# Kernel optimization log

Hardware: AMD Instinct MI355X
Metric: run time of the kernel (lower is better)

## Reference

```python
import jax, jax.numpy as jnp
import numpy as np

N_V, N_E, N_F = 6000, 12000, 8000
D_IN, D_OUT = 32, 32


def _glorot(key, shape):
    lim = float(np.sqrt(6.0 / (shape[0] + shape[1])))
    return jax.random.uniform(key, shape, jnp.float32, -lim, lim)


def setup_inputs() -> dict:
    key = jax.random.key(0)
    ks = jax.random.split(key, 13)
    return {
        "xv": jax.random.normal(ks[0], (N_V, D_IN), jnp.float32),
        "xe": jax.random.normal(ks[1], (N_E, D_IN), jnp.float32),
        "xf": jax.random.normal(ks[2], (N_F, D_IN), jnp.float32),
        "Gv2v": jax.random.normal(ks[3], (N_V, N_V), jnp.float32) / np.sqrt(N_V),
        "Gv2e": jax.random.normal(ks[4], (N_E, N_V), jnp.float32) / np.sqrt(N_V),
        "Ge2e": jax.random.normal(ks[5], (N_E, N_E), jnp.float32) / np.sqrt(N_E),
        "Ge2f": jax.random.normal(ks[6], (N_F, N_E), jnp.float32) / np.sqrt(N_E),
        "Gf2f": jax.random.normal(ks[7], (N_F, N_F), jnp.float32) / np.sqrt(N_F),
        "Wv2v": _glorot(ks[8], (D_IN, D_OUT)),
        "Wv2e": _glorot(ks[9], (D_IN, D_OUT)),
        "We2e": _glorot(ks[10], (D_IN, D_OUT)),
        "We2f": _glorot(ks[11], (D_IN, D_OUT)),
        "Wf2f": _glorot(ks[12], (D_IN, D_OUT)),
    }


def reference(xv, xe, xf, Gv2v, Gv2e, Ge2e, Ge2f, Gf2f,
              Wv2v, Wv2e, We2e, We2f, Wf2f):
    # Eval mode: dropout is identity. activation=None -> no nonlinearity.
    # LTN(x, G) = G @ (x @ W); MergeOper = sum of two LTNs.
    zv = Gv2v @ (xv @ Wv2v)                               # [n_v, d_out]
    ze = Gv2e @ (xv @ Wv2e) + Ge2e @ (xe @ We2e)          # [n_e, d_out]
    zf = Ge2f @ (xe @ We2f) + Gf2f @ (xf @ Wf2f)          # [n_f, d_out]
    return zv, ze, zf
```

## Files before the change

kernel.cpp:

```cpp
#include <hip/hip_runtime.h>

typedef float  f32x4 __attribute__((ext_vector_type(4)));
typedef short  s16x8 __attribute__((ext_vector_type(8)));

#define PK   256
#define PSTR 260

typedef const __attribute__((address_space(1))) float* gas1f;
typedef __attribute__((address_space(3))) float*       las3f;

__device__ __forceinline__ short f2bf(float f) {
  unsigned u = __builtin_bit_cast(unsigned, f);
  u += 0x7FFFu + ((u >> 16) & 1u);
  return (short)(u >> 16);
}

__global__ __launch_bounds__(256) void build_yt(
    const float* __restrict__ xv, const float* __restrict__ xe,
    const float* __restrict__ xf,
    const float* __restrict__ Wv2v, const float* __restrict__ Wv2e,
    const float* __restrict__ We2e, const float* __restrict__ We2f,
    const float* __restrict__ Wf2f, short* __restrict__ Yt)
{
  int bid = blockIdx.x;
  const float* x; const float* W; int K, Kpad; size_t yoff;
  if (bid < 24)       { x=xv; W=Wv2v; K=6000;  Kpad=6144;  yoff=0;       }
  else if (bid < 48)  { x=xv; W=Wv2e; K=6000;  Kpad=6144;  yoff=196608;  bid-=24; }
  else if (bid < 95)  { x=xe; W=We2e; K=12000; Kpad=12032; yoff=393216;  bid-=48; }
  else if (bid < 142) { x=xe; W=We2f; K=12000; Kpad=12032; yoff=778240;  bid-=95; }
  else                { x=xf; W=Wf2f; K=8000;  Kpad=8192;  yoff=1163264; bid-=142; }

  __shared__ float Wl[32][32];
  int tid = threadIdx.x;
  #pragma unroll
  for (int i = 0; i < 4; ++i) {
    int e = tid + i * 256;
    Wl[e >> 5][e & 31] = W[e];
  }
  __syncthreads();

  int row = bid * 256 + tid;
  if (row >= Kpad) return;

  float acc[32];
  #pragma unroll
  for (int c = 0; c < 32; ++c) acc[c] = 0.f;

  if (row < K) {
    const float* xp = x + (size_t)row * 32;
    float xr[32];
    #pragma unroll
    for (int i = 0; i < 8; ++i) {
      f32x4 v = *(const f32x4*)(xp + i * 4);
      xr[i*4+0] = v.x; xr[i*4+1] = v.y; xr[i*4+2] = v.z; xr[i*4+3] = v.w;
    }
    #pragma unroll
    for (int d = 0; d < 32; ++d) {
      float xd = xr[d];
      #pragma unroll
      for (int c = 0; c < 32; ++c) acc[c] += xd * Wl[d][c];
    }
  }
  #pragma unroll
  for (int c = 0; c < 32; ++c)
    Yt[yoff + (size_t)c * Kpad + row] = f2bf(acc[c]);
}

__device__ __forceinline__ void stage_panel(
    const float* __restrict__ G, int K, int row0, int pn, int lane, int w,
    float (*panel)[16][PSTR], int bb)
{
  if ((pn + 1) * PK <= K) {
    const float* base = G + (size_t)row0 * K + (size_t)pn * PK;
    #pragma unroll
    for (int j = 0; j < 4; ++j) {
      int rr = 4 * w + j;
      __builtin_amdgcn_global_load_lds((gas1f)(base + (size_t)rr * K + lane * 4),
                                       (las3f)&panel[bb][rr][0], 16, 0, 2 );
    }
  } else {
    #pragma unroll
    for (int j = 0; j < 4; ++j) {
      int rr = 4 * w + j;
      int k = pn * PK + lane * 4;
      f32x4 v = {0.f, 0.f, 0.f, 0.f};
      if (k < K) v = *(const f32x4*)(G + (size_t)(row0 + rr) * K + k);
      *(f32x4*)&panel[bb][rr][lane * 4] = v;
    }
  }
}

__device__ __forceinline__ void seg_run(
    const float* __restrict__ G, const short* __restrict__ Yt,
    int K, int Kpad, int row0, int lane, int w,
    float (*panel)[16][PSTR], f32x4& acc0, f32x4& acc1)
{
  int np = (K + PK - 1) / PK;
  int r = lane & 15, g = lane >> 4;

  stage_panel(G, K, row0, 0, lane, w, panel, 0);
  stage_panel(G, K, row0, 1, lane, w, panel, 1);

  for (int p = 0; p < np; ++p) {
    if (p + 1 < np && (p + 2) * PK <= K)
      asm volatile("s_waitcnt vmcnt(4)" ::: "memory");
    else
      asm volatile("s_waitcnt vmcnt(0)" ::: "memory");
    __builtin_amdgcn_s_barrier();

    int b = p & 1;
    #pragma unroll
    for (int si = 0; si < 2; ++si) {
      int s  = 2 * w + si;
      int kk = s * 32 + g * 8;
      f32x4 a0 = *(const f32x4*)&panel[b][r][kk];
      f32x4 a1 = *(const f32x4*)&panel[b][r][kk + 4];
      s16x8 a;
      a[0] = f2bf(a0.x); a[1] = f2bf(a0.y); a[2] = f2bf(a0.z); a[3] = f2bf(a0.w);
      a[4] = f2bf(a1.x); a[5] = f2bf(a1.y); a[6] = f2bf(a1.z); a[7] = f2bf(a1.w);
      int kg = p * PK + kk;
      s16x8 vb0 = *(const s16x8*)(Yt + (size_t)r * Kpad + kg);
      s16x8 vb1 = *(const s16x8*)(Yt + (size_t)(r + 16) * Kpad + kg);
      acc0 = __builtin_amdgcn_mfma_f32_16x16x32_bf16(a, vb0, acc0, 0, 0, 0);
      acc1 = __builtin_amdgcn_mfma_f32_16x16x32_bf16(a, vb1, acc1, 0, 0, 0);
    }

    asm volatile("s_waitcnt lgkmcnt(0)" ::: "memory");
    __builtin_amdgcn_sched_barrier(0);
    __builtin_amdgcn_s_barrier();
    if (p + 2 < np) stage_panel(G, K, row0, p + 2, lane, w, panel, b);
  }
  __syncthreads();
}

__global__ __launch_bounds__(256) void gemm_skinny(
    const float* __restrict__ Gv2v, const float* __restrict__ Gv2e,
    const float* __restrict__ Ge2e, const float* __restrict__ Ge2f,
    const float* __restrict__ Gf2f, const short* __restrict__ Yt,
    float* __restrict__ out)
{
  __shared__ float panel[2][16][PSTR];

  int bid  = blockIdx.x;
  int lane = threadIdx.x & 63, w = threadIdx.x >> 6;

  const float *G0, *G1; const short *Y0, *Y1;
  int K0, Kp0, K1, Kp1, tile; size_t ob;
  if (bid < 500) {
    tile = bid;
    G0 = Ge2f; Y0 = Yt + 778240;  K0 = 12000; Kp0 = 12032;
    G1 = Gf2f; Y1 = Yt + 1163264; K1 = 8000;  Kp1 = 8192;
    ob = (size_t)18000 * 32;
  } else if (bid < 1250) {
    tile = bid - 500;
    G0 = Gv2e; Y0 = Yt + 196608;  K0 = 6000;  Kp0 = 6144;
    G1 = Ge2e; Y1 = Yt + 393216;  K1 = 12000; Kp1 = 12032;
    ob = (size_t)6000 * 32;
  } else {
    tile = bid - 1250;
    G0 = Gv2v; Y0 = Yt;           K0 = 6000;  Kp0 = 6144;
    G1 = nullptr; Y1 = nullptr;   K1 = 0; Kp1 = 0;
    ob = 0;
  }
  int row0 = tile * 16;

  f32x4 acc0 = {0.f,0.f,0.f,0.f}, acc1 = {0.f,0.f,0.f,0.f};
  seg_run(G0, Y0, K0, Kp0, row0, lane, w, panel, acc0, acc1);
  if (G1) seg_run(G1, Y1, K1, Kp1, row0, lane, w, panel, acc0, acc1);

  float (*red)[512] = (float (*)[512])panel;
  int r = lane & 15, g = lane >> 4;
  #pragma unroll
  for (int q = 0; q < 4; ++q) {
    int rw = g * 4 + q;
    red[w][rw * 32 + r]      = acc0[q];
    red[w][rw * 32 + 16 + r] = acc1[q];
  }
  __syncthreads();
  #pragma unroll
  for (int i = 0; i < 2; ++i) {
    int e = (int)threadIdx.x + i * 256;
    float s = red[0][e] + red[1][e] + red[2][e] + red[3][e];
    out[ob + (size_t)row0 * 32 + e] = s;
  }
}

extern "C" void kernel_launch(void* const* d_in, const int* in_sizes, int n_in,
                              void* d_out, int out_size, void* d_ws, size_t ws_size,
                              hipStream_t stream) {
  const float* xv   = (const float*)d_in[0];
  const float* xe   = (const float*)d_in[1];
  const float* xf   = (const float*)d_in[2];
  const float* Gv2v = (const float*)d_in[3];
  const float* Gv2e = (const float*)d_in[4];
  const float* Ge2e = (const float*)d_in[5];
  const float* Ge2f = (const float*)d_in[6];
  const float* Gf2f = (const float*)d_in[7];
  const float* Wv2v = (const float*)d_in[8];
  const float* Wv2e = (const float*)d_in[9];
  const float* We2e = (const float*)d_in[10];
  const float* We2f = (const float*)d_in[11];
  const float* Wf2f = (const float*)d_in[12];
  short* Yt  = (short*)d_ws;
  float* out = (float*)d_out;

  hipLaunchKernelGGL(build_yt, dim3(174), dim3(256), 0, stream,
                     xv, xe, xf, Wv2v, Wv2e, We2e, We2f, Wf2f, Yt);
  hipLaunchKernelGGL(gemm_skinny, dim3(1625), dim3(256), 0, stream,
                     Gv2v, Gv2e, Ge2e, Ge2f, Gf2f, Yt, out);
}
```

Measured before the change: 356.3 us.

## Double row tile to 32 with 8 waves and prefetch B fragments a panel ahead

The skinny GEMM now gives each block 32 output rows and 512 threads, so each of the eight waves owns one 32-wide k-slice of the panel and reuses its B (Yt) fragments across two 16-row MFMA tiles. This halves the number of Yt reads from global/L2 per G row and halves the block count. B fragments for the next panel are loaded into registers one iteration ahead so they overlap the barrier and staging. The final Gv2v tile is clamped so it overlaps the previous one and rewrites identical rows. Larger blocks use more LDS and registers, which may lower occupancy, and the kernel stays dominated by streaming the fp32 G matrices.

```diff
diff --git a/kernel.cpp b/kernel.cpp
--- a/kernel.cpp
+++ b/kernel.cpp
@@ -5,6 +5,7 @@
 
 #define PK   256
 #define PSTR 260
+#define TM   32
 
 typedef const __attribute__((address_space(1))) float* gas1f;
 typedef __attribute__((address_space(3))) float*       las3f;
@@ -68,7 +69,7 @@
 
 __device__ __forceinline__ void stage_panel(
     const float* __restrict__ G, int K, int row0, int pn, int lane, int w,
-    float (*panel)[16][PSTR], int bb)
+    float (*panel)[TM][PSTR], int bb)
 {
   if ((pn + 1) * PK <= K) {
     const float* base = G + (size_t)row0 * K + (size_t)pn * PK;
@@ -90,16 +91,26 @@
   }
 }
 
+__device__ __forceinline__ void loadB(const short* __restrict__ Y, int Kp,
+                                      int r, int g, int w, int p, s16x8 B[2])
+{
+  int kg = p * PK + w * 32 + g * 8;
+  B[0] = *(const s16x8*)(Y + (size_t)r        * Kp + kg);
+  B[1] = *(const s16x8*)(Y + (size_t)(r + 16) * Kp + kg);
+}
+
 __device__ __forceinline__ void seg_run(
     const float* __restrict__ G, const short* __restrict__ Yt,
-    int K, int Kpad, int row0, int lane, int w,
-    float (*panel)[16][PSTR], f32x4& acc0, f32x4& acc1)
-{
-  int np = (K + PK - 1) / PK;
+    int K, int Kp, int np, int row0, int lane, int w,
+    float (*panel)[TM][PSTR],
+    f32x4& acc00, f32x4& acc01, f32x4& acc10, f32x4& acc11)
+{
   int r = lane & 15, g = lane >> 4;
+  s16x8 Bc[2], Bn[2];
 
   stage_panel(G, K, row0, 0, lane, w, panel, 0);
-  stage_panel(G, K, row0, 1, lane, w, panel, 1);
+  loadB(Yt, Kp, r, g, w, 0, Bc);
+  if (np > 1) stage_panel(G, K, row0, 1, lane, w, panel, 1);
 
   for (int p = 0; p < np; ++p) {
     if (p + 1 < np && (p + 2) * PK <= K)
@@ -108,79 +119,89 @@
       asm volatile("s_waitcnt vmcnt(0)" ::: "memory");
     __builtin_amdgcn_s_barrier();
 
-    int b = p & 1;
-    #pragma unroll
-    for (int si = 0; si < 2; ++si) {
-      int s  = 2 * w + si;
-      int kk = s * 32 + g * 8;
-      f32x4 a0 = *(const f32x4*)&panel[b][r][kk];
-      f32x4 a1 = *(const f32x4*)&panel[b][r][kk + 4];
-      s16x8 a;
-      a[0] = f2bf(a0.x); a[1] = f2bf(a0.y); a[2] = f2bf(a0.z); a[3] = f2bf(a0.w);
-      a[4] = f2bf(a1.x); a[5] = f2bf(a1.y); a[6] = f2bf(a1.z); a[7] = f2bf(a1.w);
-      int kg = p * PK + kk;
-      s16x8 vb0 = *(const s16x8*)(Yt + (size_t)r * Kpad + kg);
-      s16x8 vb1 = *(const s16x8*)(Yt + (size_t)(r + 16) * Kpad + kg);
-      acc0 = __builtin_amdgcn_mfma_f32_16x16x32_bf16(a, vb0, acc0, 0, 0, 0);
-      acc1 = __builtin_amdgcn_mfma_f32_16x16x32_bf16(a, vb1, acc1, 0, 0, 0);
-    }
+    int b  = p & 1;
+    int kk = w * 32 + g * 8;
+    f32x4 l0 = *(const f32x4*)&panel[b][r][kk];
+    f32x4 l1 = *(const f32x4*)&panel[b][r][kk + 4];
+    f32x4 h0 = *(const f32x4*)&panel[b][r + 16][kk];
+    f32x4 h1 = *(const f32x4*)&panel[b][r + 16][kk + 4];
+    s16x8 alo, ahi;
+    alo[0]=f2bf(l0.x); alo[1]=f2bf(l0.y); alo[2]=f2bf(l0.z); alo[3]=f2bf(l0.w);
+    alo[4]=f2bf(l1.x); alo[5]=f2bf(l1.y); alo[6]=f2bf(l1.z); alo[7]=f2bf(l1.w);
+    ahi[0]=f2bf(h0.x); ahi[1]=f2bf(h0.y); ahi[2]=f2bf(h0.z); ahi[3]=f2bf(h0.w);
+    ahi[4]=f2bf(h1.x); ahi[5]=f2bf(h1.y); ahi[6]=f2bf(h1.z); ahi[7]=f2bf(h1.w);
+    acc00 = __builtin_amdgcn_mfma_f32_16x16x32_bf16(alo, Bc[0], acc00, 0, 0, 0);
+    acc01 = __builtin_amdgcn_mfma_f32_16x16x32_bf16(alo, Bc[1], acc01, 0, 0, 0);
+    acc10 = __builtin_amdgcn_mfma_f32_16x16x32_bf16(ahi, Bc[0], acc10, 0, 0, 0);
+    acc11 = __builtin_amdgcn_mfma_f32_16x16x32_bf16(ahi, Bc[1], acc11, 0, 0, 0);
+
+    bool have_next = (p + 1 < np);
+    if (have_next) loadB(Yt, Kp, r, g, w, p + 1, Bn);
 
     asm volatile("s_waitcnt lgkmcnt(0)" ::: "memory");
     __builtin_amdgcn_sched_barrier(0);
     __builtin_amdgcn_s_barrier();
     if (p + 2 < np) stage_panel(G, K, row0, p + 2, lane, w, panel, b);
+
+    if (have_next) { Bc[0] = Bn[0]; Bc[1] = Bn[1]; }
   }
   __syncthreads();
 }
 
-__global__ __launch_bounds__(256) void gemm_skinny(
+__global__ __launch_bounds__(512) void gemm_skinny(
     const float* __restrict__ Gv2v, const float* __restrict__ Gv2e,
     const float* __restrict__ Ge2e, const float* __restrict__ Ge2f,
     const float* __restrict__ Gf2f, const short* __restrict__ Yt,
     float* __restrict__ out)
 {
-  __shared__ float panel[2][16][PSTR];
+  __shared__ float panel[2][TM][PSTR];
 
   int bid  = blockIdx.x;
   int lane = threadIdx.x & 63, w = threadIdx.x >> 6;
 
   const float *G0, *G1; const short *Y0, *Y1;
-  int K0, Kp0, K1, Kp1, tile; size_t ob;
-  if (bid < 500) {
+  int K0, Kp0, n0, K1, Kp1, n1, tile; size_t ob;
+  if (bid < 250) {
     tile = bid;
-    G0 = Ge2f; Y0 = Yt + 778240;  K0 = 12000; Kp0 = 12032;
-    G1 = Gf2f; Y1 = Yt + 1163264; K1 = 8000;  Kp1 = 8192;
-    ob = (size_t)18000 * 32;
-  } else if (bid < 1250) {
-    tile = bid - 500;
-    G0 = Gv2e; Y0 = Yt + 196608;  K0 = 6000;  Kp0 = 6144;
-    G1 = Ge2e; Y1 = Yt + 393216;  K1 = 12000; Kp1 = 12032;
-    ob = (size_t)6000 * 32;
+    G0 = Ge2f; Y0 = Yt + 778240;  K0 = 12000; Kp0 = 12032; n0 = 47;
+    G1 = Gf2f; Y1 = Yt + 1163264; K1 = 8000;  Kp1 = 8192;  n1 = 32;
+    ob = 576000;
+  } else if (bid < 625) {
+    tile = bid - 250;
+    G0 = Gv2e; Y0 = Yt + 196608;  K0 = 6000;  Kp0 = 6144;  n0 = 24;
+    G1 = Ge2e; Y1 = Yt + 393216;  K1 = 12000; Kp1 = 12032; n1 = 47;
+    ob = 192000;
   } else {
-    tile = bid - 1250;
-    G0 = Gv2v; Y0 = Yt;           K0 = 6000;  Kp0 = 6144;
-    G1 = nullptr; Y1 = nullptr;   K1 = 0; Kp1 = 0;
+    tile = bid - 625;
+    G0 = Gv2v; Y0 = Yt;           K0 = 6000;  Kp0 = 6144;  n0 = 24;
+    G1 = nullptr; Y1 = nullptr;   K1 = 0; Kp1 = 0; n1 = 0;
     ob = 0;
   }
-  int row0 = tile * 16;
-
-  f32x4 acc0 = {0.f,0.f,0.f,0.f}, acc1 = {0.f,0.f,0.f,0.f};
-  seg_run(G0, Y0, K0, Kp0, row0, lane, w, panel, acc0, acc1);
-  if (G1) seg_run(G1, Y1, K1, Kp1, row0, lane, w, panel, acc0, acc1);
-
-  float (*red)[512] = (float (*)[512])panel;
+  int row0 = tile * TM;
+  if (!G1 && row0 + TM > 6000) row0 = 6000 - TM;
+
+  f32x4 acc00 = {0.f,0.f,0.f,0.f}, acc01 = {0.f,0.f,0.f,0.f};
+  f32x4 acc10 = {0.f,0.f,0.f,0.f}, acc11 = {0.f,0.f,0.f,0.f};
+  seg_run(G0, Y0, K0, Kp0, n0, row0, lane, w, panel, acc00, acc01, acc10, acc11);
+  if (G1)
+    seg_run(G1, Y1, K1, Kp1, n1, row0, lane, w, panel, acc00, acc01, acc10, acc11);
+
+  float (*red)[1024] = (float (*)[1024])panel;
   int r = lane & 15, g = lane >> 4;
   #pragma unroll
   for (int q = 0; q < 4; ++q) {
-    int rw = g * 4 + q;
-    red[w][rw * 32 + r]      = acc0[q];
-    red[w][rw * 32 + 16 + r] = acc1[q];
+    int rl = g * 4 + q;
+    red[w][ rl       * 32 +      r] = acc00[q];
+    red[w][ rl       * 32 + 16 + r] = acc01[q];
+    red[w][(rl + 16) * 32 +      r] = acc10[q];
+    red[w][(rl + 16) * 32 + 16 + r] = acc11[q];
   }
   __syncthreads();
   #pragma unroll
   for (int i = 0; i < 2; ++i) {
-    int e = (int)threadIdx.x + i * 256;
-    float s = red[0][e] + red[1][e] + red[2][e] + red[3][e];
+    int e = (int)threadIdx.x + i * 512;
+    float s = red[0][e] + red[1][e] + red[2][e] + red[3][e]
+            + red[4][e] + red[5][e] + red[6][e] + red[7][e];
     out[ob + (size_t)row0 * 32 + e] = s;
   }
 }
@@ -206,6 +227,6 @@
 
   hipLaunchKernelGGL(build_yt, dim3(174), dim3(256), 0, stream,
                      xv, xe, xf, Wv2v, Wv2e, We2e, We2f, Wf2f, Yt);
-  hipLaunchKernelGGL(gemm_skinny, dim3(1625), dim3(256), 0, stream,
+  hipLaunchKernelGGL(gemm_skinny, dim3(813), dim3(512), 0, stream,
                      Gv2v, Gv2e, Ge2e, Ge2f, Gf2f, Yt, out);
 }
```

New measurement: 316.5 us. -11.2%, faster.
